# Optimization experiments

Hardware: AMD Instinct MI355X
Metric: run time of the kernel (lower is better)

The kernel has to match this reference:

```python
import jax, jax.numpy as jnp
import numpy as np

K = 4          # temporal_depth
IN_SIZE = 1024 # conv input channels
DN = ('NCDHW', 'OIDHW', 'NCDHW')


def setup_inputs() -> dict:
    key = jax.random.key(0)
    ks = jax.random.split(key, 12)
    B, T, C, H, W = 1, 8, IN_SIZE, 14, 14
    s = 0.02
    return {
        'videos': jax.random.normal(ks[0], (B, T, C, H, W), dtype=jnp.float32),
        # Conv3d(in_size, in_size, 3, padding='same')
        'conv1_w': jax.random.normal(ks[1], (IN_SIZE, IN_SIZE, 3, 3, 3), dtype=jnp.float32) * s,
        'conv1_b': jax.random.normal(ks[2], (IN_SIZE,), dtype=jnp.float32) * s,
        # Conv3d(in_size, 512, 3, padding='same')
        'conv2_w': jax.random.normal(ks[3], (512, IN_SIZE, 3, 3, 3), dtype=jnp.float32) * s,
        'conv2_b': jax.random.normal(ks[4], (512,), dtype=jnp.float32) * s,
        # Linear(512,512) -> Linear(512,512) -> Linear(512,128), torch (out,in) layout
        'l1_w': jax.random.normal(ks[5], (512, 512), dtype=jnp.float32) * s,
        'l1_b': jax.random.normal(ks[6], (512,), dtype=jnp.float32) * s,
        'l2_w': jax.random.normal(ks[7], (512, 512), dtype=jnp.float32) * s,
        'l2_b': jax.random.normal(ks[8], (512,), dtype=jnp.float32) * s,
        'l3_w': jax.random.normal(ks[9], (128, 512), dtype=jnp.float32) * s,
        'l3_b': jax.random.normal(ks[10], (128,), dtype=jnp.float32) * s,
    }


def reference(videos, conv1_w, conv1_b, conv2_w, conv2_b,
              l1_w, l1_b, l2_w, l2_b, l3_w, l3_b):
    B, T, C, H, W = videos.shape
    # prepend k zero frames, as in the torch code
    padded = jnp.concatenate(
        [jnp.zeros((B, K, C, H, W), videos.dtype), videos], axis=1)
    # window o covers padded frames [o, o+K) -> strictly-past original frames
    idx = jnp.arange(T)[:, None] + jnp.arange(K)[None, :]      # (T, K)
    win = padded[:, idx]                                        # (B, T, K, C, H, W)
    # permute(1,0,2,3): channels first, depth=K -> batch all windows together
    win = win.transpose(0, 1, 3, 2, 4, 5).reshape(B * T, C, K, H, W)
    # Conv3d + ReLU + Conv3d + ReLU, each with 'same' zero padding per window
    h = jax.lax.conv_general_dilated(win, conv1_w, (1, 1, 1), 'SAME',
                                     dimension_numbers=DN)
    h = jax.nn.relu(h + conv1_b[None, :, None, None, None])
    h = jax.lax.conv_general_dilated(h, conv2_w, (1, 1, 1), 'SAME',
                                     dimension_numbers=DN)
    h = jax.nn.relu(h + conv2_b[None, :, None, None, None])
    # MaxPool3d over the full (D,H,W) extent == global max per channel
    pooled = jnp.max(h, axis=(2, 3, 4))                         # (B*T, 512)
    x = jax.nn.relu(pooled @ l1_w.T + l1_b)
    x = jax.nn.relu(x @ l2_w.T + l2_b)
    x = jax.nn.relu(x @ l3_w.T + l3_b)                          # (B*T, 128)
    return x.reshape(B, T, 128)
```

## Files before the change

### kernel.cpp

```cpp
#include <hip/hip_runtime.h>

typedef __attribute__((ext_vector_type(8))) short short8;
typedef __attribute__((ext_vector_type(4))) int int4v;
typedef __attribute__((ext_vector_type(4))) float floatx4;
typedef __attribute__((ext_vector_type(4))) unsigned short ushort4v;

#define DEV __device__ __forceinline__

constexpr int M_TOT = 6272;
constexpr int M_PAD = 6400;

DEV void async_ld16(const void* g, void* l) {
  __builtin_amdgcn_global_load_lds(
      (const __attribute__((address_space(1))) unsigned int*)g,
      (__attribute__((address_space(3))) unsigned int*)l,
      16, 0, 0);
}

DEV unsigned short f2bf(float x) {
  union { float f; unsigned int u; } v; v.f = x;
  unsigned int u = v.u;
  u += 0x7FFFu + ((u >> 16) & 1u);
  return (unsigned short)(u >> 16);
}

DEV float bf2f(unsigned short s) {
  union { unsigned int u; float f; } v; v.u = ((unsigned int)s) << 16;
  return v.f;
}

struct Sched { unsigned v[256]; int n; };
struct NsTab { unsigned char v[25]; };

constexpr void cell_kdv(bool conv1, int x2, bool kdv[3]) {
  const int m0 = x2 * 256;
  const int cA = m0 / 196;
  int cB = (m0 + 255) / 196; if (cB > 31) cB = 31;
  for (int c = cA; c <= cB; ++c) {
    int t = c >> 2, d = c & 3;
    for (int kd = 0; kd < 3; ++kd) {
      int s = d + kd;
      bool ok = (s >= 1 && s <= 4);
      if (conv1) ok = ok && (s >= 5 - t);
      kdv[kd] = kdv[kd] || ok;
    }
  }
}

constexpr Sched mk_sched(bool conv1) {
  Sched out{};
  const int nt = conv1 ? 4 : 2;
  unsigned L[256] = {};
  int cnt = 0;
  for (int n = 0; n < nt; ++n) {
    for (int x2 = 0; x2 < 25; ++x2) {
      bool kdv[3] = {false, false, false};
      cell_kdv(conv1, x2, kdv);
      int vt[27] = {}; int nv = 0;
      for (int tp = 0; tp < 27; ++tp) if (kdv[tp / 9]) vt[nv++] = tp;
      if (!nv) continue;
      const int ns = conv1 ? (nv / 9) : ((nv == 27) ? 5 : 4);
      for (int s = 0; s < ns; ++s) {
        int b0 = nv * s / ns, b1 = nv * (s + 1) / ns;
        int tp0 = vt[b0], tp1 = vt[b1 - 1] + 1;
        L[cnt++] = (unsigned)(x2 | (n << 5) | (s << 7) | (tp0 << 10) | (tp1 << 15));
      }
    }
  }
  const int q = cnt / 8, r = cnt % 8;
  int pos = 0;
  for (int b = 0; b < 8; ++b) {
    const int nb = q + (b < r ? 1 : 0);
    for (int j = 0; j < nb; ++j) out.v[j * 8 + b] = L[pos++];
  }
  out.n = cnt;
  return out;
}

constexpr NsTab mk_ns(bool conv1) {
  NsTab t{};
  for (int x2 = 0; x2 < 25; ++x2) {
    bool kdv[3] = {false, false, false};
    cell_kdv(conv1, x2, kdv);
    int nv = 0;
    for (int tp = 0; tp < 27; ++tp) if (kdv[tp / 9]) ++nv;
    t.v[x2] = (nv == 0) ? 0 : (unsigned char)(conv1 ? (nv / 9) : ((nv == 27) ? 5 : 4));
  }
  return t;
}

constexpr Sched S1h = mk_sched(true);
constexpr Sched S2h = mk_sched(false);
__constant__ Sched dS1 = mk_sched(true);
__constant__ Sched dS2 = mk_sched(false);
__constant__ NsTab dNS1 = mk_ns(true);
__constant__ NsTab dNS2 = mk_ns(false);

__global__ void wtrans(const float* __restrict__ w, unsigned short* __restrict__ wt,
                       int total ) {
  __shared__ unsigned short l[256 * 27];
  const int tid  = threadIdx.x;
  const int base = blockIdx.x * 256;
  #pragma unroll 1
  for (int j = tid; j < 256 * 27; j += 256)
    l[j] = f2bf(w[(size_t)base * 27 + j]);
  __syncthreads();
  #pragma unroll 1
  for (int tap = 0; tap < 27; ++tap)
    wt[(size_t)tap * total + base + tid] = l[tid * 27 + tap];
}

__global__ void build_P1(const float* __restrict__ videos, unsigned short* __restrict__ P1) {
  const int f  = blockIdx.x;
  const int c0 = blockIdx.y * 64;
  const int tid = threadIdx.x;
  __shared__ unsigned short tile[64][196];

  #pragma unroll 1
  for (int it = 0; it < 49; ++it) {
    int idx = it * 256 + tid;
    int c = idx / 196, r = idx - c * 196;
    tile[c][r] = f2bf(videos[(size_t)(f * 1024 + c0 + c) * 196 + r]);
  }
  __syncthreads();

  const int c   = tid & 63;
  const int hwq = tid >> 6;
  #pragma unroll 1
  for (int s = 1; s <= 4; ++s) {
    int t = f + 5 - s;
    if (t > 7) continue;
    unsigned short* dst = P1 + (size_t)(t * 6 + s) * 256 * 1024 + (size_t)c0;
    #pragma unroll 1
    for (int it = 0; it < 49; ++it) {
      int hw = it * 4 + hwq;
      int h = hw / 14, w = hw - h * 14;
      dst[(size_t)((h + 1) * 16 + (w + 1)) * 1024 + c] = tile[c][hw];
    }
  }
}

#define DSR(dst, addr, off) \
  asm volatile("ds_read_b128 %0, %1 offset:" #off : "=&v"(dst) : "v"(addr))
#define WAITL(n) \
  asm volatile("s_waitcnt lgkmcnt(" #n ")" ::: "memory"); \
  __builtin_amdgcn_sched_barrier(0)
#define SB0 __builtin_amdgcn_sched_barrier(0)

template <int COUT, bool TCOND>
__global__ __launch_bounds__(512, 2) void conv_gemm(
    const unsigned short* __restrict__ P,
    const unsigned short* __restrict__ Wt,
    unsigned short* __restrict__ part)
{
  constexpr int CIN = 1024;
  __shared__ short lA[4][8192];
  __shared__ short lB[4][8192];
  const int tid  = threadIdx.x;
  const int wave = tid >> 6;
  const int lane = tid & 63;

  const unsigned int e = (TCOND ? dS1 : dS2).v[blockIdx.x];
  const int x2   = e & 31;
  const int nidx = (e >> 5) & 3;
  const int zs   = (e >> 7) & 7;
  const int tap0 = (e >> 10) & 31;
  const int tap1 = (e >> 15) & 31;
  const int m0 = x2 * 256;
  const int n0 = nidx * 256;
  unsigned short* partOut = part + (size_t)zs * M_PAD * COUT;

  bool kdv[3] = {false, false, false};
  {
    const int cA = m0 / 196;
    int cB = (m0 + 255) / 196; if (cB > 31) cB = 31;
    for (int c = cA; c <= cB; ++c) {
      int t = c >> 2, d = c & 3;
      #pragma unroll
      for (int kd = 0; kd < 3; ++kd) {
        int s = d + kd;
        bool ok = (s >= 1) && (s <= 4);
        if (TCOND) ok = ok && (s >= 5 - t);
        kdv[kd] = kdv[kd] || ok;
      }
    }
  }

  const int arow = tid >> 2;
  const int aswz = (((tid & 3) ^ ((arow >> 1) & 3)) << 4);
  int aG[2], bG[2];
  #pragma unroll
  for (int q = 0; q < 2; ++q) {
    int m = m0 + q * 128 + arow;
    int t = m / 784;  int r2 = m - t * 784;
    int d = r2 / 196; int r3 = r2 - d * 196;
    int h = r3 / 14;  int w = r3 - h * 14;
    aG[q] = ((((t * 6 + d) * 16 + h) * 16 + w) * CIN) * 2 + aswz;
    bG[q] = (n0 + q * 128 + arow) * (CIN * 2) + aswz;
  }

  int nvt = 0;
  for (int tp = tap0; tp < tap1; ++tp) if (kdv[tp / 9]) ++nvt;
  const int steps = nvt * 32;
  const char* Pb = (const char*)P;
  const char* Wb = (const char*)Wt;

  int tapS = tap0;
  while (tapS < tap1 && !kdv[tapS / 9]) ++tapS;
  int scnt = 0;
  const char *pa0 = nullptr, *pa1 = nullptr, *pb0 = nullptr, *pb1 = nullptr;
  auto tapBase = [&]() {
    const int kd = tapS / 9, rm = tapS - kd * 9;
    const int kh = rm / 3, kw = rm - kh * 3;
    const int tA = ((((kd * 16) + kh) * 16 + kw) * CIN) * 2;
    const int tB = tapS * (COUT * CIN * 2);
    pa0 = Pb + aG[0] + tA;  pa1 = Pb + aG[1] + tA;
    pb0 = Wb + bG[0] + tB;  pb1 = Wb + bG[1] + tB;
  };
  auto advS = [&]() {
    if (++scnt == 32) {
      scnt = 0;
      do { ++tapS; } while (tapS < tap1 && !kdv[tapS / 9]);
      if (tapS < tap1) tapBase();
    } else {
      pa0 += 64; pa1 += 64; pb0 += 64; pb1 += 64;
    }
  };
  tapBase();

  char* lAc = (char*)&lA[0][0];
  char* lBc = (char*)&lB[0][0];
  const unsigned ldsA0 =
      (unsigned)(size_t)(__attribute__((address_space(3))) char*)lAc;
  const unsigned ldsB0 =
      (unsigned)(size_t)(__attribute__((address_space(3))) char*)lBc;

  #pragma unroll 1
  for (int s = 0; s < 3; ++s) {
    char* dA = lAc + s * 16384;
    char* dB = lBc + s * 16384;
    async_ld16(pa0, dA + tid * 16);
    async_ld16(pb0, dB + tid * 16);
    async_ld16(pa1, dA + 8192 + tid * 16);
    async_ld16(pb1, dB + 8192 + tid * 16);
    advS();
  }
  asm volatile("s_waitcnt vmcnt(4)" ::: "memory");
  __builtin_amdgcn_s_barrier();
  SB0;

  const int wm   = (wave >> 2) * 128;
  const int wn   = (wave & 3) * 64;
  const int quad = lane >> 4;
  const int l15  = lane & 15;
  const int segc = ((quad ^ ((l15 >> 1) & 3)) << 4);
  const unsigned rowA = ((unsigned)(wm + l15) << 6) + segc;
  const unsigned rowB = ((unsigned)(wn + l15) << 6) + segc;

  floatx4 acc[8][4];
  const floatx4 zero4 = {0.f, 0.f, 0.f, 0.f};
  #pragma unroll
  for (int i = 0; i < 8; ++i)
    #pragma unroll
    for (int j = 0; j < 4; ++j) acc[i][j] = zero4;

  int4v pbE0, pbE1, pbE2, pbE3, paE0, paE1;
  int4v pbO0, pbO1, pbO2, pbO3, paO0, paO1;

  {
    const unsigned aB = ldsA0 + rowA;
    const unsigned bB = ldsB0 + rowB;
    DSR(pbE0, bB, 0);
    DSR(pbE1, bB, 1024);
    DSR(pbE2, bB, 2048);
    DSR(pbE3, bB, 3072);
    DSR(paE0, aB, 0);
    DSR(paE1, aB, 1024);
  }
  SB0;

#define MFMA_GRP(ACCI, AV)                                                  \
  {                                                                         \
    short8 a_ = __builtin_bit_cast(short8, AV);                             \
    acc[ACCI][0] = __builtin_amdgcn_mfma_f32_16x16x32_bf16(a_, bs0, acc[ACCI][0], 0, 0, 0); \
    acc[ACCI][1] = __builtin_amdgcn_mfma_f32_16x16x32_bf16(a_, bs1, acc[ACCI][1], 0, 0, 0); \
    acc[ACCI][2] = __builtin_amdgcn_mfma_f32_16x16x32_bf16(a_, bs2, acc[ACCI][2], 0, 0, 0); \
    acc[ACCI][3] = __builtin_amdgcn_mfma_f32_16x16x32_bf16(a_, bs3, acc[ACCI][3], 0, 0, 0); \
  }

#define STEP_BODY(U, PB0, PB1, PB2, PB3, PA0, PA1, NB0, NB1, NB2, NB3, NA0, NA1) \
  {                                                                         \
    const int u_ = (U);                                                     \
    const bool h3s = (u_ + 3 < steps);                                      \
    const unsigned aB = ldsA0 + (unsigned)(u_ & 3) * 16384u + rowA;         \
    int4v f2, f3, f4, f5, f6, f7;                                           \
    DSR(f2, aB, 2048);                                                      \
    DSR(f3, aB, 3072);                                                      \
    DSR(f4, aB, 4096);                                                      \
    DSR(f5, aB, 5120);                                                      \
    DSR(f6, aB, 6144);                                                      \
    DSR(f7, aB, 7168);                                                      \
    SB0;                                                                    \
    if (h3s) {                                                              \
      char* dA = lAc + ((u_ + 3) & 3) * 16384;                              \
      char* dB = lBc + ((u_ + 3) & 3) * 16384;                              \
      async_ld16(pa0, dA + tid * 16);                                       \
      async_ld16(pb0, dB + tid * 16);                                       \
      async_ld16(pa1, dA + 8192 + tid * 16);                                \
      async_ld16(pb1, dB + 8192 + tid * 16);                                \
      advS();                                                               \
    }                                                                       \
    SB0;                                                                    \
    __builtin_amdgcn_s_setprio(1);                                          \
    short8 bs0, bs1, bs2, bs3;                                              \
    WAITL(7);                                                               \
    bs0 = __builtin_bit_cast(short8, PB0);                                  \
    bs1 = __builtin_bit_cast(short8, PB1);                                  \
    bs2 = __builtin_bit_cast(short8, PB2);                                  \
    bs3 = __builtin_bit_cast(short8, PB3);                                  \
    MFMA_GRP(0, PA0);                                                       \
    WAITL(6); MFMA_GRP(1, PA1);                                             \
    WAITL(5); MFMA_GRP(2, f2);                                              \
    WAITL(4); MFMA_GRP(3, f3);                                              \
    WAITL(3); MFMA_GRP(4, f4);                                              \
    WAITL(2); MFMA_GRP(5, f5);                                              \
    WAITL(1); MFMA_GRP(6, f6);                                              \
    WAITL(0); MFMA_GRP(7, f7);                                              \
    __builtin_amdgcn_s_setprio(0);                                          \
    SB0;                                                                    \
    if (u_ + 1 < steps) {                                                   \
      const unsigned nA = ldsA0 + (unsigned)((u_ + 1) & 3) * 16384u + rowA; \
      const unsigned nB = ldsB0 + (unsigned)((u_ + 1) & 3) * 16384u + rowB; \
      DSR(NB0, nB, 0);                                                      \
      DSR(NB1, nB, 1024);                                                   \
      DSR(NB2, nB, 2048);                                                   \
      DSR(NB3, nB, 3072);                                                   \
      DSR(NA0, nA, 0);                                                      \
      DSR(NA1, nA, 1024);                                                   \
    }                                                                       \
    SB0;                                                                    \
    if (h3s) { asm volatile("s_waitcnt vmcnt(4)" ::: "memory"); }           \
    else     { asm volatile("s_waitcnt vmcnt(0)" ::: "memory"); }           \
    SB0;                                                                    \
    __builtin_amdgcn_s_barrier();                                           \
    SB0;                                                                    \
  }

  #pragma unroll 1
  for (int t = 0; t < steps; t += 2) {
    STEP_BODY(t,     pbE0, pbE1, pbE2, pbE3, paE0, paE1,
                     pbO0, pbO1, pbO2, pbO3, paO0, paO1);
    STEP_BODY(t + 1, pbO0, pbO1, pbO2, pbO3, paO0, paO1,
                     pbE0, pbE1, pbE2, pbE3, paE0, paE1);
  }

  asm volatile("s_waitcnt vmcnt(0) lgkmcnt(0)" ::: "memory");
  __builtin_amdgcn_s_barrier();

  #pragma unroll
  for (int j = 0; j < 4; ++j) {
    const int o = n0 + wn + j * 16 + l15;
    #pragma unroll
    for (int i = 0; i < 8; ++i) {
      #pragma unroll
      for (int r = 0; r < 4; ++r) {
        int m = m0 + wm + i * 16 + quad * 4 + r;
        partOut[(size_t)m * COUT + o] = f2bf(acc[i][j][r]);
      }
    }
  }
#undef STEP_BODY
#undef MFMA_GRP
}

__global__ void reduce_conv1(const unsigned short* __restrict__ part,
                             const float* __restrict__ bias,
                             unsigned short* __restrict__ P2) {
  const int m  = blockIdx.x;
  const int o4 = threadIdx.x * 4;
  const int ns = dNS1.v[m >> 8];
  const size_t ss = (size_t)M_PAD * 1024;
  const size_t base = (size_t)m * 1024 + o4;
  float v[4];
  #pragma unroll
  for (int k = 0; k < 4; ++k) v[k] = bias[o4 + k];
  #pragma unroll 1
  for (int z = 0; z < ns; ++z) {
    ushort4v p = *(const ushort4v*)(part + (size_t)z * ss + base);
    #pragma unroll
    for (int k = 0; k < 4; ++k) v[k] += bf2f(p[k]);
  }
  ushort4v out;
  #pragma unroll
  for (int k = 0; k < 4; ++k) out[k] = f2bf(v[k] > 0.f ? v[k] : 0.f);
  int t = m / 784;  int r2 = m - t * 784;
  int d = r2 / 196; int r3 = r2 - d * 196;
  int h = r3 / 14;  int w = r3 - h * 14;
  size_t didx = (size_t)(((t * 6 + d + 1) * 16 + (h + 1)) * 16 + (w + 1)) * 1024 + o4;
  *(ushort4v*)(P2 + didx) = out;
}

__global__ void reduce_conv2(const unsigned short* __restrict__ part,
                             const float* __restrict__ bias,
                             unsigned short* __restrict__ h2) {
  const int idx = blockIdx.x * 256 + threadIdx.x;
  const int m  = idx >> 7;
  const int o4 = (idx & 127) * 4;
  const int ns = dNS2.v[m >> 8];
  const size_t base = (size_t)m * 512 + o4;
  const size_t ss = (size_t)M_PAD * 512;
  float acc[4];
  #pragma unroll
  for (int k = 0; k < 4; ++k) acc[k] = bias[o4 + k];
  #pragma unroll 1
  for (int s = 0; s < ns; ++s) {
    ushort4v p = *(const ushort4v*)(part + (size_t)s * ss + base);
    #pragma unroll
    for (int k = 0; k < 4; ++k) acc[k] += bf2f(p[k]);
  }
  ushort4v out;
  #pragma unroll
  for (int k = 0; k < 4; ++k) out[k] = f2bf(acc[k] > 0.f ? acc[k] : 0.f);
  *(ushort4v*)(h2 + base) = out;
}

__global__ void pool1(const unsigned short* __restrict__ h2,
                      unsigned short* __restrict__ partial) {
  const int t = blockIdx.x / 28, ch = blockIdx.x % 28, o = threadIdx.x;
  const unsigned short* src = h2 + ((size_t)t * 784 + ch * 28) * 512 + o;
  unsigned short m = 0;
  #pragma unroll 4
  for (int i = 0; i < 28; ++i) { unsigned short v = src[(size_t)i * 512]; m = v > m ? v : m; }
  partial[((size_t)t * 28 + ch) * 512 + o] = m;
}

__global__ void mlp_kernel(const unsigned short* __restrict__ ppart,
                           const float* __restrict__ w1, const float* __restrict__ b1,
                           const float* __restrict__ w2, const float* __restrict__ b2,
                           const float* __restrict__ w3, const float* __restrict__ b3,
                           float* __restrict__ out) {
  const int t = blockIdx.x, j = threadIdx.x;
  __shared__ float xa[512], xb[512];
  {
    const unsigned short* src = ppart + (size_t)t * 28 * 512 + j;
    unsigned short m = 0;
    #pragma unroll 4
    for (int i = 0; i < 28; ++i) { unsigned short v = src[(size_t)i * 512]; m = v > m ? v : m; }
    xa[j] = bf2f(m);
  }
  __syncthreads();
  {
    const float4* wr = (const float4*)(w1 + (size_t)j * 512);
    float s = b1[j];
    #pragma unroll 4
    for (int k = 0; k < 128; ++k) {
      float4 wv = wr[k];
      s += wv.x * xa[4*k] + wv.y * xa[4*k+1] + wv.z * xa[4*k+2] + wv.w * xa[4*k+3];
    }
    xb[j] = fmaxf(s, 0.f);
  }
  __syncthreads();
  {
    const float4* wr = (const float4*)(w2 + (size_t)j * 512);
    float s = b2[j];
    #pragma unroll 4
    for (int k = 0; k < 128; ++k) {
      float4 wv = wr[k];
      s += wv.x * xb[4*k] + wv.y * xb[4*k+1] + wv.z * xb[4*k+2] + wv.w * xb[4*k+3];
    }
    xa[j] = fmaxf(s, 0.f);
  }
  __syncthreads();
  if (j < 128) {
    const float4* wr = (const float4*)(w3 + (size_t)j * 512);
    float s = b3[j];
    #pragma unroll 4
    for (int k = 0; k < 128; ++k) {
      float4 wv = wr[k];
      s += wv.x * xa[4*k] + wv.y * xa[4*k+1] + wv.z * xa[4*k+2] + wv.w * xa[4*k+3];
    }
    out[t * 128 + j] = fmaxf(s, 0.f);
  }
}

extern "C" void kernel_launch(void* const* d_in, const int* in_sizes, int n_in,
                              void* d_out, int out_size, void* d_ws, size_t ws_size,
                              hipStream_t stream) {
  const float* videos = (const float*)d_in[0];
  const float* c1w = (const float*)d_in[1];
  const float* c1b = (const float*)d_in[2];
  const float* c2w = (const float*)d_in[3];
  const float* c2b = (const float*)d_in[4];
  const float* l1w = (const float*)d_in[5];
  const float* l1b = (const float*)d_in[6];
  const float* l2w = (const float*)d_in[7];
  const float* l2b = (const float*)d_in[8];
  const float* l3w = (const float*)d_in[9];
  const float* l3b = (const float*)d_in[10];

  char* ws = (char*)d_ws;
  unsigned short* P12   = (unsigned short*)(ws);
  unsigned short* W1t   = (unsigned short*)(ws + 26738688);
  unsigned short* W2t   = (unsigned short*)(ws + 26738688);
  unsigned short* h2    = (unsigned short*)(ws + 55050240);
  unsigned short* ppart = (unsigned short*)(ws + 61489152);
  unsigned short* part  = (unsigned short*)(ws + 83361792);
  float* out = (float*)d_out;

  hipMemsetAsync(ws, 0, 26738688, stream);

  wtrans<<<4096, 256, 0, stream>>>(c1w, W1t, 1024 * 1024);
  build_P1<<<dim3(8, 16), 256, 0, stream>>>(videos, P12);

  conv_gemm<1024, true ><<<S1h.n, 512, 0, stream>>>(P12, W1t, part);

  wtrans<<<2048, 256, 0, stream>>>(c2w, W2t, 512 * 1024);
  reduce_conv1<<<6272, 256, 0, stream>>>(part, c1b, P12);

  conv_gemm<512, false><<<S2h.n, 512, 0, stream>>>(P12, W2t, part);
  reduce_conv2<<<3136, 256, 0, stream>>>(part, c2b, h2);

  pool1<<<224, 512, 0, stream>>>(h2, ppart);
  mlp_kernel<<<8, 512, 0, stream>>>(ppart, l1w, l1b, l2w, l2b, l3w, l3b, out);
}
```

Measured before the change: 746.1 us.

## Balance split-K units, merge prep kernels, split MLP into parallel layers

Split-K slices for the conv GEMMs are now divided by K-step units rather than whole taps, so slices get more even work and the per-block tap walk starts at an arbitrary step offset. The weight transpose is merged with P1 construction, and with the conv1 reduction, into single launches so the independent work shares one grid. The MLP is split into three kernels with more blocks to spread the weight reads across more CUs, at the cost of extra launches and global round-trips for intermediates.

```diff
diff --git a/kernel.cpp b/kernel.cpp
--- a/kernel.cpp
+++ b/kernel.cpp
@@ -56,14 +56,17 @@
     for (int x2 = 0; x2 < 25; ++x2) {
       bool kdv[3] = {false, false, false};
       cell_kdv(conv1, x2, kdv);
-      int vt[27] = {}; int nv = 0;
-      for (int tp = 0; tp < 27; ++tp) if (kdv[tp / 9]) vt[nv++] = tp;
+      int nv = 0;
+      for (int tp = 0; tp < 27; ++tp) if (kdv[tp / 9]) ++nv;
       if (!nv) continue;
+      const int units = nv * 32;
       const int ns = conv1 ? (nv / 9) : ((nv == 27) ? 5 : 4);
+      int bnd[8] = {};
+      bnd[0] = 0; bnd[ns] = units;
+      for (int s = 1; s < ns; ++s) bnd[s] = ((units * s / ns) + 1) & ~1;
       for (int s = 0; s < ns; ++s) {
-        int b0 = nv * s / ns, b1 = nv * (s + 1) / ns;
-        int tp0 = vt[b0], tp1 = vt[b1 - 1] + 1;
-        L[cnt++] = (unsigned)(x2 | (n << 5) | (s << 7) | (tp0 << 10) | (tp1 << 15));
+        const int su = bnd[s], c = bnd[s + 1] - bnd[s];
+        L[cnt++] = (unsigned)(x2 | (n << 5) | (s << 7) | (su << 10) | (c << 20));
       }
     }
   }
@@ -96,47 +99,87 @@
 __constant__ NsTab dNS1 = mk_ns(true);
 __constant__ NsTab dNS2 = mk_ns(false);
 
-__global__ void wtrans(const float* __restrict__ w, unsigned short* __restrict__ wt,
-                       int total ) {
+__global__ __launch_bounds__(256) void prep1(
+    const float* __restrict__ w, unsigned short* __restrict__ wt,
+    const float* __restrict__ videos, unsigned short* __restrict__ P1) {
   __shared__ unsigned short l[256 * 27];
-  const int tid  = threadIdx.x;
-  const int base = blockIdx.x * 256;
-  #pragma unroll 1
-  for (int j = tid; j < 256 * 27; j += 256)
-    l[j] = f2bf(w[(size_t)base * 27 + j]);
-  __syncthreads();
-  #pragma unroll 1
-  for (int tap = 0; tap < 27; ++tap)
-    wt[(size_t)tap * total + base + tid] = l[tid * 27 + tap];
-}
-
-__global__ void build_P1(const float* __restrict__ videos, unsigned short* __restrict__ P1) {
-  const int f  = blockIdx.x;
-  const int c0 = blockIdx.y * 64;
+  __shared__ unsigned short tile[64][196];
   const int tid = threadIdx.x;
-  __shared__ unsigned short tile[64][196];
-
-  #pragma unroll 1
-  for (int it = 0; it < 49; ++it) {
-    int idx = it * 256 + tid;
-    int c = idx / 196, r = idx - c * 196;
-    tile[c][r] = f2bf(videos[(size_t)(f * 1024 + c0 + c) * 196 + r]);
-  }
-  __syncthreads();
-
-  const int c   = tid & 63;
-  const int hwq = tid >> 6;
-  #pragma unroll 1
-  for (int s = 1; s <= 4; ++s) {
-    int t = f + 5 - s;
-    if (t > 7) continue;
-    unsigned short* dst = P1 + (size_t)(t * 6 + s) * 256 * 1024 + (size_t)c0;
+  if (blockIdx.x < 4096) {
+    const int base = blockIdx.x * 256;
+    #pragma unroll 1
+    for (int j = tid; j < 256 * 27; j += 256)
+      l[j] = f2bf(w[(size_t)base * 27 + j]);
+    __syncthreads();
+    #pragma unroll 1
+    for (int tap = 0; tap < 27; ++tap)
+      wt[(size_t)tap * (1024 * 1024) + base + tid] = l[tid * 27 + tap];
+  } else {
+    const int idx = blockIdx.x - 4096;
+    const int f  = idx >> 4;
+    const int c0 = (idx & 15) * 64;
     #pragma unroll 1
     for (int it = 0; it < 49; ++it) {
-      int hw = it * 4 + hwq;
-      int h = hw / 14, w = hw - h * 14;
-      dst[(size_t)((h + 1) * 16 + (w + 1)) * 1024 + c] = tile[c][hw];
-    }
+      int j = it * 256 + tid;
+      int c = j / 196, r = j - c * 196;
+      tile[c][r] = f2bf(videos[(size_t)(f * 1024 + c0 + c) * 196 + r]);
+    }
+    __syncthreads();
+    const int c   = tid & 63;
+    const int hwq = tid >> 6;
+    #pragma unroll 1
+    for (int s = 1; s <= 4; ++s) {
+      int t = f + 5 - s;
+      if (t > 7) continue;
+      unsigned short* dst = P1 + (size_t)(t * 6 + s) * 256 * 1024 + (size_t)c0;
+      #pragma unroll 1
+      for (int it = 0; it < 49; ++it) {
+        int hw = it * 4 + hwq;
+        int h = hw / 14, w2 = hw - h * 14;
+        dst[(size_t)((h + 1) * 16 + (w2 + 1)) * 1024 + c] = tile[c][hw];
+      }
+    }
+  }
+}
+
+__global__ __launch_bounds__(256) void prep2(
+    const float* __restrict__ w, unsigned short* __restrict__ wt,
+    const unsigned short* __restrict__ part, const float* __restrict__ bias,
+    unsigned short* __restrict__ P2) {
+  __shared__ unsigned short l[256 * 27];
+  const int tid = threadIdx.x;
+  if (blockIdx.x < 2048) {
+    const int base = blockIdx.x * 256;
+    #pragma unroll 1
+    for (int j = tid; j < 256 * 27; j += 256)
+      l[j] = f2bf(w[(size_t)base * 27 + j]);
+    __syncthreads();
+    #pragma unroll 1
+    for (int tap = 0; tap < 27; ++tap)
+      wt[(size_t)tap * (512 * 1024) + base + tid] = l[tid * 27 + tap];
+  } else {
+    const int m  = blockIdx.x - 2048;
+    const int o4 = tid * 4;
+    const int ns = dNS1.v[m >> 8];
+    const size_t ss = (size_t)M_PAD * 1024;
+    const size_t base = (size_t)m * 1024 + o4;
+    float v[4];
+    #pragma unroll
+    for (int k = 0; k < 4; ++k) v[k] = bias[o4 + k];
+    #pragma unroll 1
+    for (int z = 0; z < ns; ++z) {
+      ushort4v p = *(const ushort4v*)(part + (size_t)z * ss + base);
+      #pragma unroll
+      for (int k = 0; k < 4; ++k) v[k] += bf2f(p[k]);
+    }
+    ushort4v out;
+    #pragma unroll
+    for (int k = 0; k < 4; ++k) out[k] = f2bf(v[k] > 0.f ? v[k] : 0.f);
+    int t = m / 784;  int r2 = m - t * 784;
+    int d = r2 / 196; int r3 = r2 - d * 196;
+    int h = r3 / 14;  int w2 = r3 - h * 14;
+    size_t didx = (size_t)(((t * 6 + d + 1) * 16 + (h + 1)) * 16 + (w2 + 1)) * 1024 + o4;
+    *(ushort4v*)(P2 + didx) = out;
   }
 }
 
@@ -164,8 +207,8 @@
   const int x2   = e & 31;
   const int nidx = (e >> 5) & 3;
   const int zs   = (e >> 7) & 7;
-  const int tap0 = (e >> 10) & 31;
-  const int tap1 = (e >> 15) & 31;
+  const int su   = (e >> 10) & 1023;
+  const int steps = (e >> 20) & 1023;
   const int m0 = x2 * 256;
   const int n0 = nidx * 256;
   unsigned short* partOut = part + (size_t)zs * M_PAD * COUT;
@@ -199,15 +242,16 @@
     bG[q] = (n0 + q * 128 + arow) * (CIN * 2) + aswz;
   }
 
-  int nvt = 0;
-  for (int tp = tap0; tp < tap1; ++tp) if (kdv[tp / 9]) ++nvt;
-  const int steps = nvt * 32;
   const char* Pb = (const char*)P;
   const char* Wb = (const char*)Wt;
 
-  int tapS = tap0;
-  while (tapS < tap1 && !kdv[tapS / 9]) ++tapS;
-  int scnt = 0;
+  int tapS = 0;
+  {
+    int need = su >> 5;
+    while (!kdv[tapS / 9]) ++tapS;
+    while (need--) { do { ++tapS; } while (!kdv[tapS / 9]); }
+  }
+  int scnt = su & 31;
   const char *pa0 = nullptr, *pa1 = nullptr, *pb0 = nullptr, *pb1 = nullptr;
   auto tapBase = [&]() {
     const int kd = tapS / 9, rm = tapS - kd * 9;
@@ -217,16 +261,17 @@
     pa0 = Pb + aG[0] + tA;  pa1 = Pb + aG[1] + tA;
     pb0 = Wb + bG[0] + tB;  pb1 = Wb + bG[1] + tB;
   };
+  tapBase();
+  pa0 += scnt * 64; pa1 += scnt * 64; pb0 += scnt * 64; pb1 += scnt * 64;
   auto advS = [&]() {
     if (++scnt == 32) {
       scnt = 0;
-      do { ++tapS; } while (tapS < tap1 && !kdv[tapS / 9]);
-      if (tapS < tap1) tapBase();
+      do { ++tapS; } while (tapS < 27 && !kdv[tapS / 9]);
+      if (tapS < 27) tapBase();
     } else {
       pa0 += 64; pa1 += 64; pb0 += 64; pb1 += 64;
     }
   };
-  tapBase();
 
   char* lAc = (char*)&lA[0][0];
   char* lBc = (char*)&lB[0][0];
@@ -373,33 +418,6 @@
 #undef MFMA_GRP
 }
 
-__global__ void reduce_conv1(const unsigned short* __restrict__ part,
-                             const float* __restrict__ bias,
-                             unsigned short* __restrict__ P2) {
-  const int m  = blockIdx.x;
-  const int o4 = threadIdx.x * 4;
-  const int ns = dNS1.v[m >> 8];
-  const size_t ss = (size_t)M_PAD * 1024;
-  const size_t base = (size_t)m * 1024 + o4;
-  float v[4];
-  #pragma unroll
-  for (int k = 0; k < 4; ++k) v[k] = bias[o4 + k];
-  #pragma unroll 1
-  for (int z = 0; z < ns; ++z) {
-    ushort4v p = *(const ushort4v*)(part + (size_t)z * ss + base);
-    #pragma unroll
-    for (int k = 0; k < 4; ++k) v[k] += bf2f(p[k]);
-  }
-  ushort4v out;
-  #pragma unroll
-  for (int k = 0; k < 4; ++k) out[k] = f2bf(v[k] > 0.f ? v[k] : 0.f);
-  int t = m / 784;  int r2 = m - t * 784;
-  int d = r2 / 196; int r3 = r2 - d * 196;
-  int h = r3 / 14;  int w = r3 - h * 14;
-  size_t didx = (size_t)(((t * 6 + d + 1) * 16 + (h + 1)) * 16 + (w + 1)) * 1024 + o4;
-  *(ushort4v*)(P2 + didx) = out;
-}
-
 __global__ void reduce_conv2(const unsigned short* __restrict__ part,
                              const float* __restrict__ bias,
                              unsigned short* __restrict__ h2) {
@@ -434,53 +452,76 @@
   partial[((size_t)t * 28 + ch) * 512 + o] = m;
 }
 
-__global__ void mlp_kernel(const unsigned short* __restrict__ ppart,
-                           const float* __restrict__ w1, const float* __restrict__ b1,
-                           const float* __restrict__ w2, const float* __restrict__ b2,
-                           const float* __restrict__ w3, const float* __restrict__ b3,
-                           float* __restrict__ out) {
-  const int t = blockIdx.x, j = threadIdx.x;
-  __shared__ float xa[512], xb[512];
-  {
-    const unsigned short* src = ppart + (size_t)t * 28 * 512 + j;
+__global__ __launch_bounds__(128) void mlp_l1(
+    const unsigned short* __restrict__ ppart,
+    const float* __restrict__ w1, const float* __restrict__ b1,
+    float* __restrict__ h1) {
+  const int t = blockIdx.x >> 2, jc = blockIdx.x & 3, tid = threadIdx.x;
+  __shared__ float xa[512];
+  #pragma unroll
+  for (int q = 0; q < 4; ++q) {
+    const int c = tid * 4 + q;
+    const unsigned short* src = ppart + (size_t)t * 28 * 512 + c;
     unsigned short m = 0;
     #pragma unroll 4
     for (int i = 0; i < 28; ++i) { unsigned short v = src[(size_t)i * 512]; m = v > m ? v : m; }
-    xa[j] = bf2f(m);
+    xa[c] = bf2f(m);
   }
   __syncthreads();
-  {
-    const float4* wr = (const float4*)(w1 + (size_t)j * 512);
-    float s = b1[j];
-    #pragma unroll 4
-    for (int k = 0; k < 128; ++k) {
-      float4 wv = wr[k];
-      s += wv.x * xa[4*k] + wv.y * xa[4*k+1] + wv.z * xa[4*k+2] + wv.w * xa[4*k+3];
-    }
-    xb[j] = fmaxf(s, 0.f);
+  const int j = jc * 128 + tid;
+  const float4* wr = (const float4*)(w1 + (size_t)j * 512);
+  float s = b1[j];
+  #pragma unroll 4
+  for (int k = 0; k < 128; ++k) {
+    float4 wv = wr[k];
+    s += wv.x * xa[4*k] + wv.y * xa[4*k+1] + wv.z * xa[4*k+2] + wv.w * xa[4*k+3];
+  }
+  h1[t * 512 + j] = fmaxf(s, 0.f);
+}
+
+__global__ __launch_bounds__(128) void mlp_l2(
+    const float* __restrict__ h1,
+    const float* __restrict__ w2, const float* __restrict__ b2,
+    float* __restrict__ h2o) {
+  const int t = blockIdx.x >> 2, jc = blockIdx.x & 3, tid = threadIdx.x;
+  __shared__ float xa[512];
+  #pragma unroll
+  for (int q = 0; q < 4; ++q) {
+    const int c = tid * 4 + q;
+    xa[c] = h1[t * 512 + c];
   }
   __syncthreads();
-  {
-    const float4* wr = (const float4*)(w2 + (size_t)j * 512);
-    float s = b2[j];
-    #pragma unroll 4
-    for (int k = 0; k < 128; ++k) {
-      float4 wv = wr[k];
-      s += wv.x * xb[4*k] + wv.y * xb[4*k+1] + wv.z * xb[4*k+2] + wv.w * xb[4*k+3];
-    }
-    xa[j] = fmaxf(s, 0.f);
+  const int j = jc * 128 + tid;
+  const float4* wr = (const float4*)(w2 + (size_t)j * 512);
+  float s = b2[j];
+  #pragma unroll 4
+  for (int k = 0; k < 128; ++k) {
+    float4 wv = wr[k];
+    s += wv.x * xa[4*k] + wv.y * xa[4*k+1] + wv.z * xa[4*k+2] + wv.w * xa[4*k+3];
+  }
+  h2o[t * 512 + j] = fmaxf(s, 0.f);
+}
+
+__global__ __launch_bounds__(128) void mlp_l3(
+    const float* __restrict__ h2o,
+    const float* __restrict__ w3, const float* __restrict__ b3,
+    float* __restrict__ out) {
+  const int t = blockIdx.x, tid = threadIdx.x;
+  __shared__ float xa[512];
+  #pragma unroll
+  for (int q = 0; q < 4; ++q) {
+    const int c = tid * 4 + q;
+    xa[c] = h2o[t * 512 + c];
   }
   __syncthreads();
-  if (j < 128) {
-    const float4* wr = (const float4*)(w3 + (size_t)j * 512);
-    float s = b3[j];
-    #pragma unroll 4
-    for (int k = 0; k < 128; ++k) {
-      float4 wv = wr[k];
-      s += wv.x * xa[4*k] + wv.y * xa[4*k+1] + wv.z * xa[4*k+2] + wv.w * xa[4*k+3];
-    }
-    out[t * 128 + j] = fmaxf(s, 0.f);
-  }
+  const float4* wr = (const float4*)(w3 + (size_t)tid * 512);
+  float s = b3[tid];
+  #pragma unroll 4
+  for (int k = 0; k < 128; ++k) {
+    float4 wv = wr[k];
+    s += wv.x * xa[4*k] + wv.y * xa[4*k+1] + wv.z * xa[4*k+2] + wv.w * xa[4*k+3];
+  }
+  out[t * 128 + tid] = fmaxf(s, 0.f);
 }
 
 extern "C" void kernel_launch(void* const* d_in, const int* in_sizes, int n_in,
@@ -504,22 +545,23 @@
   unsigned short* W2t   = (unsigned short*)(ws + 26738688);
   unsigned short* h2    = (unsigned short*)(ws + 55050240);
   unsigned short* ppart = (unsigned short*)(ws + 61489152);
+  float*          mlpA  = (float*)(ws + 61718528);
+  float*          mlpB  = (float*)(ws + 61734912);
   unsigned short* part  = (unsigned short*)(ws + 83361792);
   float* out = (float*)d_out;
 
   hipMemsetAsync(ws, 0, 26738688, stream);
 
-  wtrans<<<4096, 256, 0, stream>>>(c1w, W1t, 1024 * 1024);
-  build_P1<<<dim3(8, 16), 256, 0, stream>>>(videos, P12);
-
+  prep1<<<4224, 256, 0, stream>>>(c1w, W1t, videos, P12);
   conv_gemm<1024, true ><<<S1h.n, 512, 0, stream>>>(P12, W1t, part);
 
-  wtrans<<<2048, 256, 0, stream>>>(c2w, W2t, 512 * 1024);
-  reduce_conv1<<<6272, 256, 0, stream>>>(part, c1b, P12);
+  prep2<<<8320, 256, 0, stream>>>(c2w, W2t, part, c1b, P12);
 
   conv_gemm<512, false><<<S2h.n, 512, 0, stream>>>(P12, W2t, part);
   reduce_conv2<<<3136, 256, 0, stream>>>(part, c2b, h2);
 
   pool1<<<224, 512, 0, stream>>>(h2, ppart);
-  mlp_kernel<<<8, 512, 0, stream>>>(ppart, l1w, l1b, l2w, l2b, l3w, l3b, out);
-}
+  mlp_l1<<<32, 128, 0, stream>>>(ppart, l1w, l1b, mlpA);
+  mlp_l2<<<32, 128, 0, stream>>>(mlpA, l2w, l2b, mlpB);
+  mlp_l3<<<8, 128, 0, stream>>>(mlpB, l3w, l3b, out);
+}
```

After: 689.6 us. 1.08x faster.
